# Performance work log

Measured on AMD Instinct MI355X. Metric: run time of the kernel, lower is better.

## Reference

```python
import jax, jax.numpy as jnp
import numpy as np

B, S, H = 2, 2048, 2048
N_HEADS = 16
HEAD_DIM = H // N_HEADS  # 128


def apply_rotary(x, cos, sin):
    # x: (B, n_heads, S, head_dim); cos/sin: (S, head_dim//2)
    d = x.shape[-1] // 2
    x1, x2 = x[..., :d], x[..., d:]
    c = cos[None, None, :x.shape[2]]
    s = sin[None, None, :x.shape[2]]
    return jnp.concatenate([x1 * c - x2 * s, x2 * c + x1 * s], axis=-1)


def setup_inputs() -> dict:
    key = jax.random.key(0)
    k1, k2, k3 = jax.random.split(key, 3)
    x = jax.random.normal(k1, (B, S, H), dtype=jnp.float32)
    qkv_w = jax.random.normal(k2, (3 * H, H), dtype=jnp.float32) * (1.0 / np.sqrt(H))
    o_w = jax.random.normal(k3, (H, H), dtype=jnp.float32) * (1.0 / np.sqrt(H))
    # rotary tables, half head_dim
    inv_freq = 1.0 / (10000.0 ** (jnp.arange(0, HEAD_DIM // 2, dtype=jnp.float32) / (HEAD_DIM // 2)))
    t = jnp.arange(S, dtype=jnp.float32)
    freqs = jnp.outer(t, inv_freq)  # (S, head_dim//2)
    cos, sin = jnp.cos(freqs), jnp.sin(freqs)
    # True = masked (strictly upper triangular)
    causal_mask = jnp.triu(jnp.ones((S, S), dtype=bool), k=1)
    return {"x": x, "qkv_w": qkv_w, "o_w": o_w, "cos": cos, "sin": sin,
            "causal_mask": causal_mask}


def reference(x, qkv_w, o_w, cos, sin, causal_mask):
    Bx, Sx, Hx = x.shape
    qkv = jnp.einsum('bsh,oh->bso', x, qkv_w)  # (B,S,3H)
    qkv = qkv.reshape(Bx, Sx, 3, N_HEADS, HEAD_DIM)
    q, k, v = qkv[:, :, 0], qkv[:, :, 1], qkv[:, :, 2]
    q = jnp.transpose(q, (0, 2, 1, 3))  # (B,nh,S,hd)
    k = jnp.transpose(k, (0, 2, 1, 3))
    v = jnp.transpose(v, (0, 2, 1, 3))
    q = apply_rotary(q, cos, sin)
    k = apply_rotary(k, cos, sin)
    scale = 1.0 / jnp.sqrt(jnp.asarray(HEAD_DIM, dtype=x.dtype))
    attn = jnp.einsum('bnqd,bnkd->bnqk', q, k) * scale
    attn = jnp.where(causal_mask[None, None], -jnp.inf, attn)
    attn = jax.nn.softmax(attn, axis=-1)
    out = jnp.einsum('bnqk,bnkd->bnqd', attn, v)
    out = jnp.transpose(out, (0, 2, 1, 3)).reshape(Bx, Sx, Hx)
    return jnp.einsum('bsh,oh->bso', out, o_w)
```

## Files before the change

kernel.cpp:

```cpp
#include <hip/hip_runtime.h>
#include <hip/hip_bf16.h>
#include <stdint.h>

typedef __attribute__((ext_vector_type(4))) float f32x4;
typedef __attribute__((ext_vector_type(8))) short s16x8;
typedef __attribute__((ext_vector_type(4))) short s16x4;

#define SWZ(g, row) ((((g) & ~7) | (((g) ^ ((row) & 7)) & 7)))

__device__ __forceinline__ unsigned short f2bf(float f) {
  unsigned u = __builtin_bit_cast(unsigned, f);
  u += 0x7fffu + ((u >> 16) & 1u);
  return (unsigned short)(u >> 16);
}

__device__ __forceinline__ void gld16(const void* g, void* l) {
  __builtin_amdgcn_global_load_lds(
      (const __attribute__((address_space(1))) void*)g,
      (__attribute__((address_space(3))) void*)l, 16, 0, 0);
}

__global__ void cvt_all(const float* __restrict__ x, const float* __restrict__ qkvw,
                        const float* __restrict__ ow, unsigned short* __restrict__ X16,
                        unsigned short* __restrict__ W16, unsigned short* __restrict__ OW16) {
  int i = blockIdx.x * blockDim.x + threadIdx.x;
  const float* src; unsigned short* dst; int off;
  if (i < 2097152)      { src = x;    dst = X16;  off = i; }
  else if (i < 5242880) { src = qkvw; dst = W16;  off = i - 2097152; }
  else                  { src = ow;   dst = OW16; off = i - 5242880; }
  float4 v = ((const float4*)src)[off];
  s16x4 o;
  o[0] = (short)f2bf(v.x); o[1] = (short)f2bf(v.y);
  o[2] = (short)f2bf(v.z); o[3] = (short)f2bf(v.w);
  ((s16x4*)dst)[off] = o;
}

#define PH_PRE \
  __builtin_amdgcn_s_barrier(); \
  asm volatile("s_waitcnt lgkmcnt(0)" ::: "memory"); \
  __builtin_amdgcn_sched_barrier(0); \
  __builtin_amdgcn_s_setprio(1);

#define PH_POST_N \
  __builtin_amdgcn_s_setprio(0); \
  __builtin_amdgcn_s_barrier();

#define PH_POST_W0 \
  __builtin_amdgcn_s_setprio(0); \
  asm volatile("s_waitcnt vmcnt(0)" ::: "memory"); \
  __builtin_amdgcn_s_barrier();

#define PH_POST_W2 \
  __builtin_amdgcn_s_setprio(0); \
  asm volatile("s_waitcnt vmcnt(2)" ::: "memory"); \
  __builtin_amdgcn_s_barrier();

#define PH_POST_W3 \
  __builtin_amdgcn_s_setprio(0); \
  asm volatile("s_waitcnt vmcnt(3)" ::: "memory"); \
  __builtin_amdgcn_s_barrier();

#define RDA(KS) \
  _Pragma("unroll") for (int j = 0; j < 4; ++j) { \
    const int ra = wm * 64 + j * 16 + lg; \
    av[j] = *(const s16x8*)(sA + ra * 128 + (SWZ(4 * (KS) + hg, ra) << 4)); }

#define STG_A(DST, ORG, KT) \
  _Pragma("unroll") for (int rr = 0; rr < 2; ++rr) { \
    const int G = rr * 512 + tid; const int row = G >> 3, g = G & 7; \
    gld16((const char*)((ORG) + (size_t)row * 2048 + (size_t)(KT) * 64) + (SWZ(g, row) << 4), \
          (DST) + rr * 8192 + tid * 16); }

#define STG_B2(DST, ORG, KT, R0) \
  _Pragma("unroll") for (int rr = (R0); rr < (R0) + 2; ++rr) { \
    const int G = rr * 512 + tid; const int row = G >> 3, g = G & 7; \
    gld16((const char*)((ORG) + (size_t)row * 2048 + (size_t)(KT) * 64) + (SWZ(g, row) << 4), \
          (DST) + rr * 8192 + tid * 16); }

#define RDB(KS, CH) \
  _Pragma("unroll") for (int b = 0; b < 3; ++b) { \
    const int bb = (CH) * 3 + b; \
    const int cb = (bb >> 1) * 128 + wn * 16 + (bb & 1) * 64 + lg; \
    bv[b] = *(const s16x8*)(sB + cb * 128 + (SWZ(4 * (KS) + hg, cb) << 4)); }

#define MM12(CH) \
  _Pragma("unroll") for (int j = 0; j < 4; ++j) \
    _Pragma("unroll") for (int b = 0; b < 3; ++b) \
      acc[j][(CH) * 3 + b] = __builtin_amdgcn_mfma_f32_16x16x32_bf16( \
          av[j], bv[b], acc[j][(CH) * 3 + b], 0, 0, 0);

__global__ __launch_bounds__(512, 1) void gemm_qkv_384(
    const unsigned short* __restrict__ A,
    const unsigned short* __restrict__ Bt,
    const float* __restrict__ cosT, const float* __restrict__ sinT,
    unsigned short* __restrict__ qOut, unsigned short* __restrict__ kOut,
    unsigned short* __restrict__ vtOut)
{
  __shared__ char smem[131072];
  const int tid = (int)threadIdx.x;
  const int wid = tid >> 6, l = tid & 63;
  const int lg = l & 15, hg = l >> 4;
  const int wm = wid >> 2, wn = wid & 3;
  const int s = ((int)blockIdx.x & 7) * 64 + ((int)blockIdx.x >> 3);
  const int bm0 = (s & 31) * 128, bn0 = (s >> 5) * 384;

  const unsigned short* Aorg = A + (size_t)bm0 * 2048;
  const unsigned short* Borg = Bt + (size_t)bn0 * 2048;

  f32x4 acc[4][6] = {};

  STG_A(smem + 0, Aorg, 0)
  STG_B2(smem + 16384, Borg, 0, 0)
  STG_B2(smem + 16384, Borg, 0, 2)
  STG_B2(smem + 16384, Borg, 0, 4)
  asm volatile("s_waitcnt vmcnt(3)" ::: "memory");
  __builtin_amdgcn_s_barrier();

  for (int t = 0; t < 31; ++t) {
    const char* sA = smem + (t & 1) * 65536;
    const char* sB = sA + 16384;
    char* dA = smem + ((t & 1) ^ 1) * 65536;
    char* dB = dA + 16384;
    s16x8 av[4], bv[3];
    RDA(0) RDB(0, 0) STG_A(dA, Aorg, t + 1)      PH_PRE MM12(0) PH_POST_W2
    RDB(0, 1)        STG_B2(dB, Borg, t + 1, 0)  PH_PRE MM12(1) PH_POST_N
    RDA(1) RDB(1, 1) STG_B2(dB, Borg, t + 1, 2)  PH_PRE MM12(1) PH_POST_N
    RDB(1, 0)        STG_B2(dB, Borg, t + 1, 4)  PH_PRE MM12(0) PH_POST_W3
  }
  {
    const char* sA = smem + 65536;
    const char* sB = sA + 16384;
    s16x8 av[4], bv[3];
    RDA(0) RDB(0, 0)  PH_PRE MM12(0) PH_POST_W0
    RDB(0, 1)         PH_PRE MM12(1) PH_POST_N
    RDA(1) RDB(1, 1)  PH_PRE MM12(1) PH_POST_N
    RDB(1, 0)         PH_PRE MM12(0)
    __builtin_amdgcn_s_setprio(0);
  }

  #pragma unroll
  for (int j = 0; j < 4; ++j) {
    const int grow0 = bm0 + wm * 64 + j * 16 + hg * 4;
    const int b_ = grow0 >> 11;
    #pragma unroll
    for (int cg = 0; cg < 3; ++cg) {
      const int og = (bn0 >> 7) + cg;
      const int tt = og >> 4, h = og & 15;
      const int d = wn * 16 + lg;
      if (tt < 2) {
        unsigned short* dst = (tt == 0) ? qOut : kOut;
        #pragma unroll
        for (int r = 0; r < 4; ++r) {
          const int gr = grow0 + r;
          const int s1 = gr & 2047;
          const float x1 = acc[j][cg * 2 + 0][r];
          const float x2 = acc[j][cg * 2 + 1][r];
          const float cv = cosT[s1 * 64 + d];
          const float sv = sinT[s1 * 64 + d];
          const size_t base = (((size_t)b_ * 16 + h) * 2048 + s1) * 128;
          dst[base + d]      = f2bf(x1 * cv - x2 * sv);
          dst[base + d + 64] = f2bf(x2 * cv + x1 * sv);
        }
      } else {
        const int s0 = grow0 & 2047;
        s16x4 p1, p2;
        #pragma unroll
        for (int r = 0; r < 4; ++r) {
          p1[r] = (short)f2bf(acc[j][cg * 2 + 0][r]);
          p2[r] = (short)f2bf(acc[j][cg * 2 + 1][r]);
        }
        *(s16x4*)(vtOut + (((size_t)b_ * 16 + h) * 128 + d)      * 2048 + s0) = p1;
        *(s16x4*)(vtOut + (((size_t)b_ * 16 + h) * 128 + d + 64) * 2048 + s0) = p2;
      }
    }
  }
}

#define RDBO(KS, CH) \
  _Pragma("unroll") for (int b = 0; b < 2; ++b) { \
    const int cb = ((CH) * 2 + b) * 64 + wn * 16 + lg; \
    bv[b] = *(const s16x8*)(sB + cb * 128 + (SWZ(4 * (KS) + hg, cb) << 4)); }

#define MMO(CH) \
  _Pragma("unroll") for (int j = 0; j < 4; ++j) \
    _Pragma("unroll") for (int b = 0; b < 2; ++b) \
      acc[j][(CH) * 2 + b] = __builtin_amdgcn_mfma_f32_16x16x32_bf16( \
          av[j], bv[b], acc[j][(CH) * 2 + b], 0, 0, 0);

__global__ __launch_bounds__(512, 1) void gemm_op_256(
    const unsigned short* __restrict__ A,
    const unsigned short* __restrict__ Bt,
    float* __restrict__ C)
{
  __shared__ char smem[98304];
  const int tid = (int)threadIdx.x;
  const int wid = tid >> 6, l = tid & 63;
  const int lg = l & 15, hg = l >> 4;
  const int wm = wid >> 2, wn = wid & 3;
  const int s = ((int)blockIdx.x & 7) * 32 + ((int)blockIdx.x >> 3);
  const int bm0 = (s & 31) * 128, bn0 = (s >> 5) * 256;

  const unsigned short* Aorg = A + (size_t)bm0 * 2048;
  const unsigned short* Borg = Bt + (size_t)bn0 * 2048;

  f32x4 acc[4][4] = {};

  STG_A(smem + 0, Aorg, 0)
  STG_B2(smem + 16384, Borg, 0, 0)
  STG_B2(smem + 16384, Borg, 0, 2)
  asm volatile("s_waitcnt vmcnt(2)" ::: "memory");
  __builtin_amdgcn_s_barrier();

  for (int t = 0; t < 31; ++t) {
    const char* sA = smem + (t & 1) * 49152;
    const char* sB = sA + 16384;
    char* dA = smem + ((t & 1) ^ 1) * 49152;
    char* dB = dA + 16384;
    s16x8 av[4], bv[2];
    RDA(0) RDBO(0, 0) STG_A(dA, Aorg, t + 1)      PH_PRE MMO(0) PH_POST_W2
    RDBO(0, 1)        STG_B2(dB, Borg, t + 1, 0)  PH_PRE MMO(1) PH_POST_N
    RDA(1) RDBO(1, 1) STG_B2(dB, Borg, t + 1, 2)  PH_PRE MMO(1) PH_POST_N
    RDBO(1, 0)                                    PH_PRE MMO(0) PH_POST_W2
  }
  {
    const char* sA = smem + 49152;
    const char* sB = sA + 16384;
    s16x8 av[4], bv[2];
    RDA(0) RDBO(0, 0)  PH_PRE MMO(0) PH_POST_W0
    RDBO(0, 1)         PH_PRE MMO(1) PH_POST_N
    RDA(1) RDBO(1, 1)  PH_PRE MMO(1) PH_POST_N
    RDBO(1, 0)         PH_PRE MMO(0)
    __builtin_amdgcn_s_setprio(0);
  }

  #pragma unroll
  for (int j = 0; j < 4; ++j) {
    const int row0 = bm0 + wm * 64 + j * 16 + hg * 4;
    #pragma unroll
    for (int b = 0; b < 4; ++b) {
      const int col = bn0 + b * 64 + wn * 16 + lg;
      #pragma unroll
      for (int r = 0; r < 4; ++r)
        C[(size_t)(row0 + r) * 2048 + col] = acc[j][b][r];
    }
  }
}

__global__ __launch_bounds__(256) void attn_fwd(
    const unsigned short* __restrict__ Qp, const unsigned short* __restrict__ Kp,
    const unsigned short* __restrict__ Vt, unsigned short* __restrict__ AO)
{
  __shared__ char sK[16384];
  __shared__ char sV[16384];
  __shared__ char sP[8192];

  const int tid = (int)threadIdx.x, w = tid >> 6, l = tid & 63;
  const int lg = l & 15, hg = l >> 4;
  const int bid = (int)blockIdx.x;
  const int p = bid >> 8, c = bid & 255;
  const int j = c >> 5, bh = c & 31;
  const int qt = (p == 0) ? j : (p == 1) ? 31 - j : (p == 2) ? 8 + j : 23 - j;
  const size_t qkBase = (size_t)bh * 2048 * 128;
  const int qw0 = qt * 64 + w * 16;
  const int qi = qw0 + lg;

  s16x8 qf[4];
  for (int ks = 0; ks < 4; ++ks)
    qf[ks] = *(const s16x8*)(Qp + qkBase + (size_t)(qw0 + lg) * 128 + ks * 32 + hg * 8);

  f32x4 acc_o[8] = {};
  float mrun = -1e30f, lrun = 0.f;
  const float SCALE = 0.08838834764831845f;
  const float L2E = 1.4426950408889634f;
  const float CS = SCALE * L2E;

  const int nkv = qt + 1;
  for (int kv = 0; kv < nkv; ++kv) {
    const int kv0 = kv * 64;
    __syncthreads();
    for (int i = 0; i < 4; ++i) {
      const int G = w * 256 + i * 64 + l;
      const int rk = G >> 4, gk = G & 15;
      gld16((const char*)(Kp + qkBase + (size_t)(kv0 + rk) * 128) + (SWZ(gk, rk) << 4),
            sK + w * 4096 + i * 1024);
      const int rv = G >> 3, gv = G & 7;
      gld16((const char*)(Vt + qkBase + (size_t)rv * 2048 + kv0) + (SWZ(gv, rv) << 4),
            sV + w * 4096 + i * 1024);
    }
    asm volatile("s_waitcnt vmcnt(0)" ::: "memory");
    __syncthreads();

    f32x4 accs[4] = {};
    for (int ks = 0; ks < 4; ++ks)
      for (int kf = 0; kf < 4; ++kf) {
        const int row = kf * 16 + lg;
        const int g = SWZ(4 * ks + hg, row);
        s16x8 kfrag = *(const s16x8*)(sK + row * 256 + (g << 4));
        accs[kf] = __builtin_amdgcn_mfma_f32_16x16x32_bf16(kfrag, qf[ks], accs[kf], 0, 0, 0);
      }

    const bool diag = (kv == qt);
    float raw[4][4];
    float mt = -1e30f;
    #pragma unroll
    for (int kf = 0; kf < 4; ++kf)
      #pragma unroll
      for (int r = 0; r < 4; ++r) {
        float s = accs[kf][r];
        if (diag) {
          const int jj = kv0 + kf * 16 + hg * 4 + r;
          s = (jj > qi) ? -1e30f : s;
        }
        raw[kf][r] = s;
        mt = fmaxf(mt, s);
      }
    mt = fmaxf(mt, __shfl_xor(mt, 16));
    mt = fmaxf(mt, __shfl_xor(mt, 32));
    mt *= SCALE;
    if (!__all(mt - mrun <= 8.0f)) {
      const float mnew = fmaxf(mrun, mt);
      const float alpha = exp2f((mrun - mnew) * L2E);
      float ar[4];
      #pragma unroll
      for (int r = 0; r < 4; ++r) ar[r] = __shfl(alpha, hg * 4 + r);
      #pragma unroll
      for (int f = 0; f < 8; ++f)
        #pragma unroll
        for (int r = 0; r < 4; ++r) acc_o[f][r] *= ar[r];
      lrun *= alpha;
      mrun = mnew;
    }
    const float mL = mrun * L2E;
    float ls = 0.f;
    char* pw = sP + w * 2048;
    #pragma unroll
    for (int kf = 0; kf < 4; ++kf) {
      s16x4 pk;
      #pragma unroll
      for (int r = 0; r < 4; ++r) {
        const float e = exp2f(raw[kf][r] * CS - mL);
        ls += e;
        pk[r] = (short)f2bf(e);
      }
      const int j0 = kf * 16 + hg * 4;
      *(s16x4*)(pw + lg * 128 + (SWZ(j0 >> 3, lg) << 4) + ((j0 * 2) & 15)) = pk;
    }
    ls += __shfl_xor(ls, 16);
    ls += __shfl_xor(ls, 32);
    lrun += ls;
    asm volatile("" ::: "memory");

    for (int jc = 0; jc < 2; ++jc) {
      const int gp = SWZ(hg + 4 * jc, lg);
      s16x8 pa = *(const s16x8*)(pw + lg * 128 + (gp << 4));
      for (int f = 0; f < 8; ++f) {
        const int rv = f * 16 + lg;
        const int gv = SWZ(hg + 4 * jc, rv);
        s16x8 vb = *(const s16x8*)(sV + rv * 128 + (gv << 4));
        acc_o[f] = __builtin_amdgcn_mfma_f32_16x16x32_bf16(pa, vb, acc_o[f], 0, 0, 0);
      }
    }
  }

  float linv[4];
  for (int r = 0; r < 4; ++r) linv[r] = 1.0f / __shfl(lrun, hg * 4 + r);
  const int b = bh >> 4, h = bh & 15;
  for (int f = 0; f < 8; ++f) {
    const int d = h * 128 + f * 16 + lg;
    for (int r = 0; r < 4; ++r) {
      const int srow = qw0 + hg * 4 + r;
      AO[((size_t)(b * 2048 + srow)) * 2048 + d] = f2bf(acc_o[f][r] * linv[r]);
    }
  }
}

extern "C" void kernel_launch(void* const* d_in, const int* in_sizes, int n_in,
                              void* d_out, int out_size, void* d_ws, size_t ws_size,
                              hipStream_t stream) {
  const float* x    = (const float*)d_in[0];
  const float* qkvw = (const float*)d_in[1];
  const float* ow   = (const float*)d_in[2];
  const float* cosT = (const float*)d_in[3];
  const float* sinT = (const float*)d_in[4];
  float* out = (float*)d_out;

  unsigned short* X16  = (unsigned short*)d_ws;
  unsigned short* W16  = X16  + (size_t)8388608;
  unsigned short* OW16 = W16  + (size_t)12582912;
  unsigned short* Qp   = OW16 + (size_t)4194304;
  unsigned short* Kp   = Qp   + (size_t)8388608;
  unsigned short* Vtp  = Kp   + (size_t)8388608;
  unsigned short* AO   = Vtp  + (size_t)8388608;

  cvt_all<<<24576, 256, 0, stream>>>(x, qkvw, ow, X16, W16, OW16);

  gemm_qkv_384<<<512, 512, 0, stream>>>(X16, W16, cosT, sinT, Qp, Kp, Vtp);

  attn_fwd<<<1024, 256, 0, stream>>>(Qp, Kp, Vtp, AO);

  gemm_op_256<<<256, 512, 0, stream>>>(AO, OW16, out);
}
```

Measured before the change: 234.1 us.

## Prefetch next K/V tile into registers while computing current attention tile

Replaces the direct global-to-LDS loads of K and V at the top of each kv iteration with register prefetch. The next tile is loaded into registers before the QK^T and PV MFMAs run, then written to swizzled LDS after a barrier. This is meant to hide global memory latency behind compute. It costs extra VGPRs for the staging registers and adds an explicit LDS write pass, and the launch bounds now request 4 blocks per CU, which may constrain register allocation.

New measurement: 279.4 us. +19.3%, slower.

```diff
diff --git a/kernel.cpp b/kernel.cpp
--- a/kernel.cpp
+++ b/kernel.cpp
@@ -246,7 +246,25 @@
   }
 }
 
-__global__ __launch_bounds__(256) void attn_fwd(
+#define LDR(KV0) \
+  _Pragma("unroll") for (int i = 0; i < 4; ++i) { \
+    const int Gk = i * 256 + tid; \
+    kreg[i] = *(const s16x8*)(Kp + qkBase + (size_t)((KV0) + (Gk >> 4)) * 128 + (Gk & 15) * 8); \
+    const int Gv = i * 256 + tid; \
+    vreg[i] = *(const s16x8*)(Vt + qkBase + (size_t)(Gv >> 3) * 2048 + (KV0) + (Gv & 7) * 8); \
+  }
+
+#define WRS() \
+  _Pragma("unroll") for (int i = 0; i < 4; ++i) { \
+    const int Gk = i * 256 + tid; \
+    const int rk = Gk >> 4, gk = Gk & 15; \
+    *(s16x8*)(sK + rk * 256 + (SWZ(gk, rk) << 4)) = kreg[i]; \
+    const int Gv = i * 256 + tid; \
+    const int rv = Gv >> 3, gv = Gv & 7; \
+    *(s16x8*)(sV + rv * 128 + (SWZ(gv, rv) << 4)) = vreg[i]; \
+  }
+
+__global__ __launch_bounds__(256, 4) void attn_fwd(
     const unsigned short* __restrict__ Qp, const unsigned short* __restrict__ Kp,
     const unsigned short* __restrict__ Vt, unsigned short* __restrict__ AO)
 {
@@ -274,21 +292,19 @@
   const float L2E = 1.4426950408889634f;
   const float CS = SCALE * L2E;
 
+  s16x8 kreg[4], vreg[4];
+
+  LDR(0)
+  asm volatile("s_waitcnt vmcnt(0)" ::: "memory");
+  WRS()
+  asm volatile("s_waitcnt lgkmcnt(0)" ::: "memory");
+  __syncthreads();
+
   const int nkv = qt + 1;
   for (int kv = 0; kv < nkv; ++kv) {
     const int kv0 = kv * 64;
-    __syncthreads();
-    for (int i = 0; i < 4; ++i) {
-      const int G = w * 256 + i * 64 + l;
-      const int rk = G >> 4, gk = G & 15;
-      gld16((const char*)(Kp + qkBase + (size_t)(kv0 + rk) * 128) + (SWZ(gk, rk) << 4),
-            sK + w * 4096 + i * 1024);
-      const int rv = G >> 3, gv = G & 7;
-      gld16((const char*)(Vt + qkBase + (size_t)rv * 2048 + kv0) + (SWZ(gv, rv) << 4),
-            sV + w * 4096 + i * 1024);
-    }
-    asm volatile("s_waitcnt vmcnt(0)" ::: "memory");
-    __syncthreads();
+
+    if (kv + 1 < nkv) { LDR(kv0 + 64) }
 
     f32x4 accs[4] = {};
     for (int ks = 0; ks < 4; ++ks)
@@ -360,6 +376,14 @@
         acc_o[f] = __builtin_amdgcn_mfma_f32_16x16x32_bf16(pa, vb, acc_o[f], 0, 0, 0);
       }
     }
+
+    __syncthreads();
+    if (kv + 1 < nkv) {
+      asm volatile("s_waitcnt vmcnt(0)" ::: "memory");
+      WRS()
+      asm volatile("s_waitcnt lgkmcnt(0)" ::: "memory");
+    }
+    __syncthreads();
   }
 
   float linv[4];
```

## Double-buffer K/V tiles with 32-row steps and per-wave causal skipping

Applied to the files above, without the earlier changes.

Restructures the attention inner loop to process 32-key tiles and double-buffer K and V in LDS, prefetching tile kv+2 while computing tile kv, with vmcnt-based waits. The V tile layout is repacked so a 32-key slice fits the new buffer. Waves whose 16 query rows lie entirely before the tile skip its compute, which trims causal work at a finer grain. The cost is twice as many loop iterations and barriers, plus half-size MFMA batches per iteration.

Result: no change. 238.5 us (+1.8%).

```diff
diff --git a/kernel.cpp b/kernel.cpp
--- a/kernel.cpp
+++ b/kernel.cpp
@@ -246,12 +246,24 @@
   }
 }
 
+#define ASTG32(BB, KV0) \
+  _Pragma("unroll") for (int i = 0; i < 2; ++i) { \
+    const int G = i * 256 + tid; \
+    const int rk = G >> 4, gk = G & 15; \
+    gld16((const char*)(Kp + qkBase + (size_t)((KV0) + rk) * 128) + (SWZ(gk, rk) << 4), \
+          &sK[BB][(i * 4096) + (tid >> 6) * 1024 + (tid & 63) * 16]); \
+    const int rp = G >> 3, gp_ = G & 7; \
+    const int gl = SWZ(gp_, rp); \
+    gld16((const char*)(Vt + qkBase + (size_t)(rp + ((gl >> 2) << 6)) * 2048 + (KV0) + (gl & 3) * 8), \
+          &sV[BB][(i * 4096) + (tid >> 6) * 1024 + (tid & 63) * 16]); \
+  }
+
 __global__ __launch_bounds__(256) void attn_fwd(
     const unsigned short* __restrict__ Qp, const unsigned short* __restrict__ Kp,
     const unsigned short* __restrict__ Vt, unsigned short* __restrict__ AO)
 {
-  __shared__ char sK[16384];
-  __shared__ char sV[16384];
+  __shared__ char sK[2][8192];
+  __shared__ char sV[2][8192];
   __shared__ char sP[8192];
 
   const int tid = (int)threadIdx.x, w = tid >> 6, l = tid & 63;
@@ -274,92 +286,104 @@
   const float L2E = 1.4426950408889634f;
   const float CS = SCALE * L2E;
 
-  const int nkv = qt + 1;
+  const int nkv = 2 * qt + 2;
+
+  ASTG32(0, 0)
+  ASTG32(1, 32)
+  asm volatile("s_waitcnt vmcnt(4)" ::: "memory");
+  __builtin_amdgcn_s_barrier();
+
   for (int kv = 0; kv < nkv; ++kv) {
-    const int kv0 = kv * 64;
-    __syncthreads();
-    for (int i = 0; i < 4; ++i) {
-      const int G = w * 256 + i * 64 + l;
-      const int rk = G >> 4, gk = G & 15;
-      gld16((const char*)(Kp + qkBase + (size_t)(kv0 + rk) * 128) + (SWZ(gk, rk) << 4),
-            sK + w * 4096 + i * 1024);
-      const int rv = G >> 3, gv = G & 7;
-      gld16((const char*)(Vt + qkBase + (size_t)rv * 2048 + kv0) + (SWZ(gv, rv) << 4),
-            sV + w * 4096 + i * 1024);
-    }
-    asm volatile("s_waitcnt vmcnt(0)" ::: "memory");
-    __syncthreads();
-
-    f32x4 accs[4] = {};
-    for (int ks = 0; ks < 4; ++ks)
-      for (int kf = 0; kf < 4; ++kf) {
-        const int row = kf * 16 + lg;
-        const int g = SWZ(4 * ks + hg, row);
-        s16x8 kfrag = *(const s16x8*)(sK + row * 256 + (g << 4));
-        accs[kf] = __builtin_amdgcn_mfma_f32_16x16x32_bf16(kfrag, qf[ks], accs[kf], 0, 0, 0);
+    const int cur = kv & 1;
+    const int kv0 = kv * 32;
+    const char* cK = sK[cur];
+    const char* cV = sV[cur];
+    const bool act = (kv0 <= qw0 + 15);
+
+    if (act) {
+      f32x4 accs[2] = {};
+      #pragma unroll
+      for (int ks = 0; ks < 4; ++ks)
+        #pragma unroll
+        for (int kf = 0; kf < 2; ++kf) {
+          const int row = kf * 16 + lg;
+          s16x8 kfrag = *(const s16x8*)(cK + row * 256 + (SWZ(4 * ks + hg, row) << 4));
+          accs[kf] = __builtin_amdgcn_mfma_f32_16x16x32_bf16(kfrag, qf[ks], accs[kf], 0, 0, 0);
+        }
+
+      const bool diag = (kv0 + 31 > qi) || (kv0 + 31 > qw0 + 15);
+      float raw[2][4];
+      float mt = -1e30f;
+      #pragma unroll
+      for (int kf = 0; kf < 2; ++kf)
+        #pragma unroll
+        for (int r = 0; r < 4; ++r) {
+          float sv_ = accs[kf][r];
+          if (diag) {
+            const int jj = kv0 + kf * 16 + hg * 4 + r;
+            sv_ = (jj > qi) ? -1e30f : sv_;
+          }
+          raw[kf][r] = sv_;
+          mt = fmaxf(mt, sv_);
+        }
+      mt = fmaxf(mt, __shfl_xor(mt, 16));
+      mt = fmaxf(mt, __shfl_xor(mt, 32));
+      mt *= SCALE;
+      if (!__all(mt - mrun <= 8.0f)) {
+        const float mnew = fmaxf(mrun, mt);
+        const float alpha = exp2f((mrun - mnew) * L2E);
+        float ar[4];
+        #pragma unroll
+        for (int r = 0; r < 4; ++r) ar[r] = __shfl(alpha, hg * 4 + r);
+        #pragma unroll
+        for (int f = 0; f < 8; ++f)
+          #pragma unroll
+          for (int r = 0; r < 4; ++r) acc_o[f][r] *= ar[r];
+        lrun *= alpha;
+        mrun = mnew;
       }
-
-    const bool diag = (kv == qt);
-    float raw[4][4];
-    float mt = -1e30f;
-    #pragma unroll
-    for (int kf = 0; kf < 4; ++kf)
+      const float mL = mrun * L2E;
+      float ls = 0.f;
+      char* pw = sP + w * 2048;
       #pragma unroll
-      for (int r = 0; r < 4; ++r) {
-        float s = accs[kf][r];
-        if (diag) {
-          const int jj = kv0 + kf * 16 + hg * 4 + r;
-          s = (jj > qi) ? -1e30f : s;
-        }
-        raw[kf][r] = s;
-        mt = fmaxf(mt, s);
+      for (int kf = 0; kf < 2; ++kf) {
+        s16x4 pk;
+        #pragma unroll
+        for (int r = 0; r < 4; ++r) {
+          const float e = exp2f(raw[kf][r] * CS - mL);
+          ls += e;
+          pk[r] = (short)f2bf(e);
+        }
+        const int j0 = kf * 16 + hg * 4;
+        *(s16x4*)(pw + lg * 128 + (SWZ(j0 >> 3, lg) << 4) + ((j0 * 2) & 15)) = pk;
       }
-    mt = fmaxf(mt, __shfl_xor(mt, 16));
-    mt = fmaxf(mt, __shfl_xor(mt, 32));
-    mt *= SCALE;
-    if (!__all(mt - mrun <= 8.0f)) {
-      const float mnew = fmaxf(mrun, mt);
-      const float alpha = exp2f((mrun - mnew) * L2E);
-      float ar[4];
-      #pragma unroll
-      for (int r = 0; r < 4; ++r) ar[r] = __shfl(alpha, hg * 4 + r);
-      #pragma unroll
-      for (int f = 0; f < 8; ++f)
-        #pragma unroll
-        for (int r = 0; r < 4; ++r) acc_o[f][r] *= ar[r];
-      lrun *= alpha;
-      mrun = mnew;
-    }
-    const float mL = mrun * L2E;
-    float ls = 0.f;
-    char* pw = sP + w * 2048;
-    #pragma unroll
-    for (int kf = 0; kf < 4; ++kf) {
-      s16x4 pk;
-      #pragma unroll
-      for (int r = 0; r < 4; ++r) {
-        const float e = exp2f(raw[kf][r] * CS - mL);
-        ls += e;
-        pk[r] = (short)f2bf(e);
-      }
-      const int j0 = kf * 16 + hg * 4;
-      *(s16x4*)(pw + lg * 128 + (SWZ(j0 >> 3, lg) << 4) + ((j0 * 2) & 15)) = pk;
-    }
-    ls += __shfl_xor(ls, 16);
-    ls += __shfl_xor(ls, 32);
-    lrun += ls;
-    asm volatile("" ::: "memory");
-
-    for (int jc = 0; jc < 2; ++jc) {
-      const int gp = SWZ(hg + 4 * jc, lg);
-      s16x8 pa = *(const s16x8*)(pw + lg * 128 + (gp << 4));
-      for (int f = 0; f < 8; ++f) {
-        const int rv = f * 16 + lg;
-        const int gv = SWZ(hg + 4 * jc, rv);
-        s16x8 vb = *(const s16x8*)(sV + rv * 128 + (gv << 4));
-        acc_o[f] = __builtin_amdgcn_mfma_f32_16x16x32_bf16(pa, vb, acc_o[f], 0, 0, 0);
+      ls += __shfl_xor(ls, 16);
+      ls += __shfl_xor(ls, 32);
+      lrun += ls;
+      asm volatile("" ::: "memory");
+
+      {
+        const int gpn = SWZ(hg, lg);
+        s16x8 pa = *(const s16x8*)(pw + lg * 128 + (gpn << 4));
+        #pragma unroll
+        for (int f = 0; f < 8; ++f) {
+          const int d = f * 16 + lg;
+          const int rowv = d & 63;
+          const int gv = ((d >> 6) << 2) + hg;
+          s16x8 vb = *(const s16x8*)(cV + rowv * 128 + (SWZ(gv, rowv) << 4));
+          acc_o[f] = __builtin_amdgcn_mfma_f32_16x16x32_bf16(pa, vb, acc_o[f], 0, 0, 0);
+        }
       }
     }
+
+    __builtin_amdgcn_s_barrier();
+    if (kv + 2 < nkv) {
+      ASTG32(cur, kv0 + 64)
+      asm volatile("s_waitcnt vmcnt(4)" ::: "memory");
+    } else {
+      asm volatile("s_waitcnt vmcnt(0)" ::: "memory");
+    }
+    __builtin_amdgcn_s_barrier();
   }
 
   float linv[4];
```
